# Kernel tuning notes

Hardware: AMD Instinct MI355X
Metric: run time of the kernel (lower is better)

## Reference

```python
import jax, jax.numpy as jnp
import numpy as np

NUM_POINTS = 100000
BATCH = 4096
K = 10


def setup_inputs() -> dict:
    key = jax.random.key(0)
    k1, k2, k3, k4, k5 = jax.random.split(key, 5)
    rays_o = jax.random.normal(k1, (BATCH, 3), dtype=jnp.float32)
    rays_d = jax.random.normal(k2, (BATCH, 3), dtype=jnp.float32)
    xyz = jax.random.normal(k3, (NUM_POINTS, 3), dtype=jnp.float32) * 0.1
    features_dc = jax.random.normal(k4, (NUM_POINTS, 1, 3), dtype=jnp.float32)
    opacity = jax.random.normal(k5, (NUM_POINTS, 1), dtype=jnp.float32)
    return {"rays_o": rays_o, "rays_d": rays_d, "xyz": xyz,
            "features_dc": features_dc, "opacity": opacity}


def reference(rays_o, rays_d, xyz, features_dc, opacity):
    # colors = sigmoid(features[:,0,:]) ; features[:,0,:] == features_dc[:,0,:]
    colors = jax.nn.sigmoid(features_dc[:, 0, :])          # [N,3]
    op = jax.nn.sigmoid(opacity[:, 0])                      # [N]
    ray_centers = rays_o + rays_d * 3.0                     # [B,3]
    # Euclidean cdist via ||a||^2 + ||b||^2 - 2 a.b (matmul form, like torch.cdist p=2)
    sq = (jnp.sum(ray_centers * ray_centers, axis=1)[:, None]
          + jnp.sum(xyz * xyz, axis=1)[None, :]
          - 2.0 * ray_centers @ xyz.T)                      # [B,N]
    distances = jnp.sqrt(jnp.maximum(sq, 0.0))
    # top-K smallest distances per ray
    _, idx = jax.lax.top_k(-distances, K)                   # [B,K]
    d_sel = jnp.take_along_axis(distances, idx, axis=1)     # [B,K]
    w = jnp.exp(-d_sel * 0.1) * op[idx]                     # [B,K]
    w = w / (jnp.sum(w, axis=1, keepdims=True) + 1e-8)
    rgb = jnp.einsum('bk,bkc->bc', w, colors[idx])          # [B,3]
    return rgb
```

## Files before the change

kernel.cpp:

```cpp
#include <hip/hip_runtime.h>
#include <math.h>

#define NPTS   100000
#define NRAYS  4096
#define KTOP   10
#define KMER   12
#define CAP    128
#define LCAP   12

#define PPAIR  4
#define SBLK   49
#define RCS    64
#define RPBS   (NRAYS / RCS)

#define TPAIR  2
#define NPART  64
#define TRAYS  8

typedef float v2f __attribute__((ext_vector_type(2)));

static_assert(SBLK * 2048 >= NPTS, "scan covers all points");
static_assert(NPART * 256 <= NPTS, "theta sample within real points");

__device__ __forceinline__ float4 make_center(const float* __restrict__ ro,
                                              const float* __restrict__ rd,
                                              int ray, float w) {
    float ox = ro[3 * ray + 0], oy = ro[3 * ray + 1], oz = ro[3 * ray + 2];
    float dx = rd[3 * ray + 0], dy = rd[3 * ray + 1], dz = rd[3 * ray + 2];
    float cx, cy, cz;
    {
#pragma clang fp contract(off)
        cx = ox + dx * 3.0f;
        cy = oy + dy * 3.0f;
        cz = oz + dz * 3.0f;
    }
    return make_float4(cx, cy, cz, w);
}

__device__ __forceinline__ float sigm(float x) { return 1.0f / (1.0f + expf(-x)); }

__device__ __forceinline__ unsigned long long mkkey(float sc, int id, bool v) {
    unsigned u = __float_as_uint(sc);
    u = (u & 0x80000000u) ? ~u : (u | 0x80000000u);
    unsigned long long k = ((unsigned long long)u << 32) | (unsigned)(~id);
    return v ? k : 0ull;
}

__global__ __launch_bounds__(256, 2) void theta_kernel(const float* __restrict__ xyz,
                                                       const float* __restrict__ ro,
                                                       const float* __restrict__ rd,
                                                       float* __restrict__ theta,
                                                       int* __restrict__ cnt) {
    __shared__ float4 rsh[TRAYS];
    __shared__ float  pmsh[NPART][TRAYS];
    const int tid = threadIdx.x, wave = tid >> 6, lane = tid & 63;
    const int rbase = blockIdx.x * TRAYS;

    if (tid < TRAYS) rsh[tid] = make_center(ro, rd, rbase + tid, 0.0f);
    __syncthreads();

#pragma unroll 1
    for (int pi = 0; pi < NPART / 4; ++pi) {
        const int part = pi * 4 + wave;
        const int id0 = part * 256 + lane;
        v2f px[TPAIR], py[TPAIR], pz[TPAIR], pw[TPAIR];
#pragma unroll
        for (int u = 0; u < TPAIR; ++u) {
            int ia = id0 + (2 * u) * 64, ib = id0 + (2 * u + 1) * 64;
            float xa = xyz[3 * ia + 0], ya = xyz[3 * ia + 1], za = xyz[3 * ia + 2];
            float xb = xyz[3 * ib + 0], yb = xyz[3 * ib + 1], zb = xyz[3 * ib + 2];
            px[u] = (v2f){xa, xb}; py[u] = (v2f){ya, yb}; pz[u] = (v2f){za, zb};
            pw[u] = (v2f){-0.5f * fmaf(xa, xa, fmaf(ya, ya, za * za)),
                          -0.5f * fmaf(xb, xb, fmaf(yb, yb, zb * zb))};
        }
#pragma unroll
        for (int r = 0; r < TRAYS; r += 4) {
            float4 r0 = rsh[r], r1 = rsh[r + 1], r2 = rsh[r + 2], r3 = rsh[r + 3];
            v2f a0 = (v2f){-INFINITY, -INFINITY}, a1 = a0, a2 = a0, a3 = a0;
#pragma unroll
            for (int u = 0; u < TPAIR; ++u) {
                v2f t0 = __builtin_elementwise_fma(pz[u], (v2f){r0.z, r0.z}, pw[u]);
                t0 = __builtin_elementwise_fma(py[u], (v2f){r0.y, r0.y}, t0);
                t0 = __builtin_elementwise_fma(px[u], (v2f){r0.x, r0.x}, t0);
                a0 = __builtin_elementwise_max(a0, t0);
                v2f t1 = __builtin_elementwise_fma(pz[u], (v2f){r1.z, r1.z}, pw[u]);
                t1 = __builtin_elementwise_fma(py[u], (v2f){r1.y, r1.y}, t1);
                t1 = __builtin_elementwise_fma(px[u], (v2f){r1.x, r1.x}, t1);
                a1 = __builtin_elementwise_max(a1, t1);
                v2f t2 = __builtin_elementwise_fma(pz[u], (v2f){r2.z, r2.z}, pw[u]);
                t2 = __builtin_elementwise_fma(py[u], (v2f){r2.y, r2.y}, t2);
                t2 = __builtin_elementwise_fma(px[u], (v2f){r2.x, r2.x}, t2);
                a2 = __builtin_elementwise_max(a2, t2);
                v2f t3 = __builtin_elementwise_fma(pz[u], (v2f){r3.z, r3.z}, pw[u]);
                t3 = __builtin_elementwise_fma(py[u], (v2f){r3.y, r3.y}, t3);
                t3 = __builtin_elementwise_fma(px[u], (v2f){r3.x, r3.x}, t3);
                a3 = __builtin_elementwise_max(a3, t3);
            }
            float m0 = fmaxf(a0.x, a0.y), m1 = fmaxf(a1.x, a1.y);
            float m2 = fmaxf(a2.x, a2.y), m3 = fmaxf(a3.x, a3.y);
#pragma unroll
            for (int off = 1; off < 64; off <<= 1) {
                m0 = fmaxf(m0, __shfl_xor(m0, off));
                m1 = fmaxf(m1, __shfl_xor(m1, off));
                m2 = fmaxf(m2, __shfl_xor(m2, off));
                m3 = fmaxf(m3, __shfl_xor(m3, off));
            }
            if (lane == 0) {
                pmsh[part][r]     = m0;
                pmsh[part][r + 1] = m1;
                pmsh[part][r + 2] = m2;
                pmsh[part][r + 3] = m3;
            }
        }
    }

    __syncthreads();
    if (tid < TRAYS) {
        float vs[KTOP];
#pragma unroll
        for (int j = 0; j < KTOP; ++j) vs[j] = -INFINITY;
#pragma unroll 1
        for (int p = 0; p < NPART; ++p) {
            float v = pmsh[p][tid];
#pragma unroll
            for (int t = KTOP - 1; t >= 1; --t) {
                bool up = v > vs[t - 1], here = v > vs[t];
                vs[t] = up ? vs[t - 1] : (here ? v : vs[t]);
            }
            vs[0] = fmaxf(vs[0], v);
        }
        theta[rbase + tid] = vs[KTOP - 1];
        cnt[rbase + tid] = 0;
    }
}

__global__ __launch_bounds__(256) void scan_kernel(const float* __restrict__ xyz,
                                                   const float* __restrict__ ro,
                                                   const float* __restrict__ rd,
                                                   const float* __restrict__ theta,
                                                   int* __restrict__ cnt,
                                                   float2* __restrict__ cand) {
    __shared__ float4 rsh[RPBS];
    __shared__ int    lcnt[RPBS];
    __shared__ float2 lbuf[RPBS][LCAP];
    const int pblk = blockIdx.x, rchunk = blockIdx.y;
    const int tid = threadIdx.x, wave = tid >> 6, lane = tid & 63;
    const int rbase = rchunk * RPBS;

    if (tid < RPBS) {
        rsh[tid] = make_center(ro, rd, rbase + tid, theta[rbase + tid]);
        lcnt[tid] = 0;
    }

    const int id0 = pblk * 2048 + wave * 512 + lane;
    v2f px[PPAIR], py[PPAIR], pz[PPAIR], pw[PPAIR];
#pragma unroll
    for (int u = 0; u < PPAIR; ++u) {
        int ia = id0 + (2 * u) * 64, ib = id0 + (2 * u + 1) * 64;
        bool va = ia < NPTS, vb = ib < NPTS;
        int ca = va ? ia : 0, cb = vb ? ib : 0;
        float xa = xyz[3 * ca + 0], ya = xyz[3 * ca + 1], za = xyz[3 * ca + 2];
        float xb = xyz[3 * cb + 0], yb = xyz[3 * cb + 1], zb = xyz[3 * cb + 2];
        px[u] = (v2f){xa, xb}; py[u] = (v2f){ya, yb}; pz[u] = (v2f){za, zb};
        pw[u] = (v2f){va ? -0.5f * fmaf(xa, xa, fmaf(ya, ya, za * za)) : -INFINITY,
                      vb ? -0.5f * fmaf(xb, xb, fmaf(yb, yb, zb * zb)) : -INFINITY};
    }
    __syncthreads();

    auto emit = [&](int r, float sc, int id) {
        int slot = atomicAdd(&lcnt[r], 1);
        float2 e = make_float2(sc, __int_as_float(id));
        if (slot < LCAP) lbuf[r][slot] = e;
        else {
            int gs = atomicAdd(&cnt[rbase + r], 1);
            if (gs < CAP) cand[((rbase + r) << 7) + gs] = e;
        }
    };

#pragma unroll 4
    for (int r = 0; r < RPBS; ++r) {
        float4 rp = rsh[r];
        const v2f rx = (v2f){rp.x, rp.x}, ry = (v2f){rp.y, rp.y}, rz = (v2f){rp.z, rp.z};
        v2f s[PPAIR];
        v2f a0, a1;
        {
            v2f t = __builtin_elementwise_fma(pz[0], rz, pw[0]);
            t = __builtin_elementwise_fma(py[0], ry, t);
            t = __builtin_elementwise_fma(px[0], rx, t);
            s[0] = t; a0 = t;
            t = __builtin_elementwise_fma(pz[1], rz, pw[1]);
            t = __builtin_elementwise_fma(py[1], ry, t);
            t = __builtin_elementwise_fma(px[1], rx, t);
            s[1] = t; a1 = t;
            t = __builtin_elementwise_fma(pz[2], rz, pw[2]);
            t = __builtin_elementwise_fma(py[2], ry, t);
            t = __builtin_elementwise_fma(px[2], rx, t);
            s[2] = t; a0 = __builtin_elementwise_max(a0, t);
            t = __builtin_elementwise_fma(pz[3], rz, pw[3]);
            t = __builtin_elementwise_fma(py[3], ry, t);
            t = __builtin_elementwise_fma(px[3], rx, t);
            s[3] = t; a1 = __builtin_elementwise_max(a1, t);
        }
        v2f am = __builtin_elementwise_max(a0, a1);
        float hm = fmaxf(am.x, am.y);

        if (__ballot(hm >= rp.w)) {
#pragma unroll
            for (int u = 0; u < PPAIR; ++u) {
                if (__ballot(s[u].x >= rp.w)) {
                    if (s[u].x >= rp.w) emit(r, s[u].x, id0 + (2 * u) * 64);
                }
                if (__ballot(s[u].y >= rp.w)) {
                    if (s[u].y >= rp.w) emit(r, s[u].y, id0 + (2 * u + 1) * 64);
                }
            }
        }
    }

    __syncthreads();
    if (tid < RPBS) {
        int n = lcnt[tid];
        n = n < LCAP ? n : LCAP;
        if (n > 0) {
            const int rayid = rbase + tid;
            int base = atomicAdd(&cnt[rayid], n);
            for (int j = 0; j < n; ++j) {
                int slot = base + j;
                if (slot < CAP) cand[(rayid << 7) + slot] = lbuf[tid][j];
            }
        }
    }
}

__global__ __launch_bounds__(256) void merge_kernel(const float* __restrict__ ro,
                                                    const float* __restrict__ rd,
                                                    const int* __restrict__ cnt,
                                                    const float2* __restrict__ cand,
                                                    const float* __restrict__ xyz,
                                                    const float* __restrict__ fdc,
                                                    const float* __restrict__ opac,
                                                    float* __restrict__ out) {
    const int wave = threadIdx.x >> 6, lane = threadIdx.x & 63;
    const int ray = blockIdx.x * 4 + wave;

    int n = cnt[ray];
    n = n < CAP ? n : CAP;

    const float2* cl = cand + (ray << 7);
    float2 e0 = cl[lane];
    float2 e1 = cl[64 + lane];
    int id0 = __float_as_int(e0.y), id1 = __float_as_int(e1.y);

    unsigned long long k0 = mkkey(e0.x, id0, lane < n);
    unsigned long long k1 = mkkey(e1.x, id1, lane + 64 < n);

    int sel = -1;
    unsigned long long kl = k0 > k1 ? k0 : k1;
#pragma unroll
    for (int j = 0; j < KMER; ++j) {
        unsigned long long m = kl;
#pragma unroll
        for (int off = 1; off < 64; off <<= 1) {
            unsigned long long o = __shfl_xor(m, off);
            m = m > o ? m : o;
        }
        bool win = (kl == m) && (m != 0ull);
        int wid = (k0 >= k1) ? id0 : id1;
        unsigned long long wmask = __ballot(win);
        int wl = __ffsll(wmask) - 1;
        int bid = __shfl(wid, wl & 63);
        if (m == 0ull) bid = -1;
        if (lane == j) sel = bid;
        if (win) {
            if (k0 >= k1) k0 = 0ull; else k1 = 0ull;
            kl = k0 > k1 ? k0 : k1;
        }
    }

    float ox = ro[3 * ray + 0], oy = ro[3 * ray + 1], oz = ro[3 * ray + 2];
    float dx = rd[3 * ray + 0], dy = rd[3 * ray + 1], dz = rd[3 * ray + 2];
    float cxf, cyf, czf;
    {
#pragma clang fp contract(off)
        cxf = ox + dx * 3.0f;
        cyf = oy + dy * 3.0f;
        czf = oz + dz * 3.0f;
    }
    double Cx = (double)cxf, Cy = (double)cyf, Cz = (double)czf;
    double cn = Cx * Cx + Cy * Cy + Cz * Cz;

    bool valid = (lane < KMER) && (sel >= 0);
    int pid = valid ? sel : 0;
    double X = (double)xyz[3 * pid + 0];
    double Y = (double)xyz[3 * pid + 1];
    double Z = (double)xyz[3 * pid + 2];
    double sq = valid ? (cn + (X * X + Y * Y + Z * Z) - 2.0 * (Cx * X + Cy * Y + Cz * Z))
                      : (double)INFINITY;
    int cid = valid ? sel : 0x7fffffff;

    int rank = 0;
#pragma unroll
    for (int k = 0; k < KMER; ++k) {
        double sk = __shfl(sq, k);
        int    ik = __shfl(cid, k);
        if ((sk < sq) || (sk == sq && ik < cid)) ++rank;
    }

    bool take = valid && (rank < KTOP);
    float w = 0.0f, rr = 0.0f, gg = 0.0f, bb = 0.0f;
    if (take) {
        float dd = sqrtf(fmaxf((float)sq, 0.0f));
        w  = expf(-0.1f * dd) * sigm(opac[pid]);
        rr = w * sigm(fdc[3 * pid + 0]);
        gg = w * sigm(fdc[3 * pid + 1]);
        bb = w * sigm(fdc[3 * pid + 2]);
    }
#pragma unroll
    for (int off = 1; off < 64; off <<= 1) {
        w  += __shfl_xor(w,  off);
        rr += __shfl_xor(rr, off);
        gg += __shfl_xor(gg, off);
        bb += __shfl_xor(bb, off);
    }
    if (lane == 0) {
        float inv = 1.0f / (w + 1e-8f);
        out[3 * ray + 0] = rr * inv;
        out[3 * ray + 1] = gg * inv;
        out[3 * ray + 2] = bb * inv;
    }
}

extern "C" void kernel_launch(void* const* d_in, const int* in_sizes, int n_in,
                              void* d_out, int out_size, void* d_ws, size_t ws_size,
                              hipStream_t stream) {
    const float* rays_o = (const float*)d_in[0];
    const float* rays_d = (const float*)d_in[1];
    const float* xyz    = (const float*)d_in[2];
    const float* fdc    = (const float*)d_in[3];
    const float* opac   = (const float*)d_in[4];
    float* out = (float*)d_out;

    char* w = (char*)d_ws;
    float*  theta  = (float*)w;  w += (size_t)NRAYS * 4;
    int*    cnt    = (int*)w;    w += (size_t)NRAYS * 4;
    float2* cand   = (float2*)w;

    theta_kernel<<<NRAYS / TRAYS, 256, 0, stream>>>(xyz, rays_o, rays_d, theta, cnt);
    scan_kernel<<<dim3(SBLK, RCS), 256, 0, stream>>>(xyz, rays_o, rays_d, theta, cnt, cand);
    merge_kernel<<<NRAYS / 4, 256, 0, stream>>>(rays_o, rays_d, cnt, cand, xyz, fdc, opac, out);
}
```

Before: 160.6 us.

## Restructure theta partition max to per-lane accumulators, drop per-group wave shuffles

The theta kernel now keeps a running per-lane max across all sample groups in registers, one per ray, instead of doing a 64-lane shuffle reduction per partition. Partitions are redefined as strided lane sets (lane index across 4 waves and 16 groups), combined through a shared array at the end. Per-thread point batch doubles to 4 pairs per iteration. This removes many cross-lane shuffles and LDS writes in exchange for more registers. Partition membership changes, but each partition still covers disjoint real points, so the theta lower bound stays valid.

```diff
diff --git a/kernel.cpp b/kernel.cpp
--- a/kernel.cpp
+++ b/kernel.cpp
@@ -13,14 +13,15 @@
 #define RCS    64
 #define RPBS   (NRAYS / RCS)
 
-#define TPAIR  2
+#define TPAIR  4
 #define NPART  64
 #define TRAYS  8
+#define TGRP   16
 
 typedef float v2f __attribute__((ext_vector_type(2)));
 
 static_assert(SBLK * 2048 >= NPTS, "scan covers all points");
-static_assert(NPART * 256 <= NPTS, "theta sample within real points");
+static_assert(TGRP * 2048 <= NPTS, "theta sample within real points");
 
 __device__ __forceinline__ float4 make_center(const float* __restrict__ ro,
                                               const float* __restrict__ rd,
@@ -52,17 +53,24 @@
                                                        float* __restrict__ theta,
                                                        int* __restrict__ cnt) {
     __shared__ float4 rsh[TRAYS];
-    __shared__ float  pmsh[NPART][TRAYS];
+    __shared__ float  Msh[4][TRAYS][64];
     const int tid = threadIdx.x, wave = tid >> 6, lane = tid & 63;
     const int rbase = blockIdx.x * TRAYS;
 
     if (tid < TRAYS) rsh[tid] = make_center(ro, rd, rbase + tid, 0.0f);
     __syncthreads();
 
+    float4 rr[TRAYS];
+#pragma unroll
+    for (int r = 0; r < TRAYS; ++r) rr[r] = rsh[r];
+
+    v2f M[TRAYS];
+#pragma unroll
+    for (int r = 0; r < TRAYS; ++r) M[r] = (v2f){-INFINITY, -INFINITY};
+
 #pragma unroll 1
-    for (int pi = 0; pi < NPART / 4; ++pi) {
-        const int part = pi * 4 + wave;
-        const int id0 = part * 256 + lane;
+    for (int g = 0; g < TGRP; ++g) {
+        const int id0 = g * 2048 + wave * 512 + lane;
         v2f px[TPAIR], py[TPAIR], pz[TPAIR], pw[TPAIR];
 #pragma unroll
         for (int u = 0; u < TPAIR; ++u) {
@@ -74,54 +82,35 @@
                           -0.5f * fmaf(xb, xb, fmaf(yb, yb, zb * zb))};
         }
 #pragma unroll
-        for (int r = 0; r < TRAYS; r += 4) {
-            float4 r0 = rsh[r], r1 = rsh[r + 1], r2 = rsh[r + 2], r3 = rsh[r + 3];
-            v2f a0 = (v2f){-INFINITY, -INFINITY}, a1 = a0, a2 = a0, a3 = a0;
+        for (int r = 0; r < TRAYS; ++r) {
+            const v2f rx = (v2f){rr[r].x, rr[r].x};
+            const v2f ry = (v2f){rr[r].y, rr[r].y};
+            const v2f rz = (v2f){rr[r].z, rr[r].z};
+            v2f m = M[r];
 #pragma unroll
             for (int u = 0; u < TPAIR; ++u) {
-                v2f t0 = __builtin_elementwise_fma(pz[u], (v2f){r0.z, r0.z}, pw[u]);
-                t0 = __builtin_elementwise_fma(py[u], (v2f){r0.y, r0.y}, t0);
-                t0 = __builtin_elementwise_fma(px[u], (v2f){r0.x, r0.x}, t0);
-                a0 = __builtin_elementwise_max(a0, t0);
-                v2f t1 = __builtin_elementwise_fma(pz[u], (v2f){r1.z, r1.z}, pw[u]);
-                t1 = __builtin_elementwise_fma(py[u], (v2f){r1.y, r1.y}, t1);
-                t1 = __builtin_elementwise_fma(px[u], (v2f){r1.x, r1.x}, t1);
-                a1 = __builtin_elementwise_max(a1, t1);
-                v2f t2 = __builtin_elementwise_fma(pz[u], (v2f){r2.z, r2.z}, pw[u]);
-                t2 = __builtin_elementwise_fma(py[u], (v2f){r2.y, r2.y}, t2);
-                t2 = __builtin_elementwise_fma(px[u], (v2f){r2.x, r2.x}, t2);
-                a2 = __builtin_elementwise_max(a2, t2);
-                v2f t3 = __builtin_elementwise_fma(pz[u], (v2f){r3.z, r3.z}, pw[u]);
-                t3 = __builtin_elementwise_fma(py[u], (v2f){r3.y, r3.y}, t3);
-                t3 = __builtin_elementwise_fma(px[u], (v2f){r3.x, r3.x}, t3);
-                a3 = __builtin_elementwise_max(a3, t3);
+                v2f t = __builtin_elementwise_fma(pz[u], rz, pw[u]);
+                t = __builtin_elementwise_fma(py[u], ry, t);
+                t = __builtin_elementwise_fma(px[u], rx, t);
+                m = __builtin_elementwise_max(m, t);
             }
-            float m0 = fmaxf(a0.x, a0.y), m1 = fmaxf(a1.x, a1.y);
-            float m2 = fmaxf(a2.x, a2.y), m3 = fmaxf(a3.x, a3.y);
-#pragma unroll
-            for (int off = 1; off < 64; off <<= 1) {
-                m0 = fmaxf(m0, __shfl_xor(m0, off));
-                m1 = fmaxf(m1, __shfl_xor(m1, off));
-                m2 = fmaxf(m2, __shfl_xor(m2, off));
-                m3 = fmaxf(m3, __shfl_xor(m3, off));
-            }
-            if (lane == 0) {
-                pmsh[part][r]     = m0;
-                pmsh[part][r + 1] = m1;
-                pmsh[part][r + 2] = m2;
-                pmsh[part][r + 3] = m3;
-            }
-        }
-    }
-
+            M[r] = m;
+        }
+    }
+
+#pragma unroll
+    for (int r = 0; r < TRAYS; ++r)
+        Msh[wave][r][lane] = fmaxf(M[r].x, M[r].y);
     __syncthreads();
+
     if (tid < TRAYS) {
         float vs[KTOP];
 #pragma unroll
         for (int j = 0; j < KTOP; ++j) vs[j] = -INFINITY;
 #pragma unroll 1
         for (int p = 0; p < NPART; ++p) {
-            float v = pmsh[p][tid];
+            float v = fmaxf(fmaxf(Msh[0][tid][p], Msh[1][tid][p]),
+                            fmaxf(Msh[2][tid][p], Msh[3][tid][p]));
 #pragma unroll
             for (int t = KTOP - 1; t >= 1; --t) {
                 bool up = v > vs[t - 1], here = v > vs[t];
```

After: 151.5 us. 5.7% less time.
